# Kernel tuning notes

Hardware: AMD Instinct MI355X
Metric: run time of the kernel (lower is better)

## Reference

```python
import jax, jax.numpy as jnp
import numpy as np

N_ITERATIONS = 3
EPS = 1e-07


def squash(t, axis=-1):
    sqr_norm = jnp.sum(t * t, axis=axis, keepdims=True)
    norm = jnp.sqrt(sqr_norm + EPS)
    return sqr_norm * t / ((1.0 + sqr_norm) * norm)


def setup_inputs() -> dict:
    key = jax.random.key(0)
    B, N_IN, N_OUT, D = 256, 1152, 10, 16
    u_hat = jax.random.normal(key, (B, N_IN, N_OUT, D, 1), dtype=jnp.float32)
    return {"u_hat": u_hat}


def reference(u_hat):
    # u_hat: [B, n_in, n_out, d, 1]
    B, n_in, n_out = u_hat.shape[0], u_hat.shape[1], u_hat.shape[2]
    b = jnp.zeros((B, n_in, n_out, 1, 1), dtype=u_hat.dtype)
    v = None
    for r in range(N_ITERATIONS):
        c = jax.nn.softmax(b, axis=1)                      # softmax over input caps
        s = jnp.sum(c * u_hat, axis=1, keepdims=True)      # [B, 1, n_out, d, 1]
        v = squash(s, axis=-2)                             # squash over capsule dim
        if r < N_ITERATIONS - 1:
            # u_hat^T @ v (broadcast v over input caps): agreement [B, n_in, n_out, 1, 1]
            a = jnp.sum(u_hat * v, axis=-2, keepdims=True)
            b = b + a
    return jnp.squeeze(v, axis=1)                          # [B, n_out, d, 1]
```

## Files before the change

kernel.cpp:

```cpp
#include <hip/hip_runtime.h>

#define BATCH 256
#define NIN   1152
#define NOUT  10
#define DDIM  16
#define KPT   18

__global__ __launch_bounds__(256)
void routing_kernel(const float* __restrict__ u_hat, float* __restrict__ out) {
    __shared__ float bsh[NIN];
    __shared__ float wsh[NIN];
    __shared__ float red[4 * DDIM];
    __shared__ float vsh[DDIM];
    __shared__ float scal[8];

    const int t    = threadIdx.x;
    const int q    = t & 3;
    const int g    = t >> 2;
    const int wave = t >> 6;
    const int lane = t & 63;

    const int x   = blockIdx.x;
    const int xcd = x & 7;
    const int j   = x >> 3;
    const int oo  = j % NOUT;
    const int bb  = xcd * 32 + j / NOUT;

    const float* base = u_hat + (size_t)bb * (NIN * NOUT * DDIM) + oo * DDIM + q * 4;

    float4 u[KPT];
#pragma unroll
    for (int k = 0; k < KPT; ++k) {
        const int i = g + 64 * k;
        u[k] = *reinterpret_cast<const float4*>(base + (size_t)i * (NOUT * DDIM));
    }

    for (int i = t; i < NIN; i += 256) bsh[i] = 0.0f;
    __syncthreads();

    for (int r = 0; r < 3; ++r) {
        float m = -3.4e38f;
        for (int i = t; i < NIN; i += 256) m = fmaxf(m, bsh[i]);
        for (int off = 32; off >= 1; off >>= 1) m = fmaxf(m, __shfl_down(m, off));
        if (lane == 0) scal[wave] = m;
        __syncthreads();
        m = fmaxf(fmaxf(scal[0], scal[1]), fmaxf(scal[2], scal[3]));

        float z = 0.0f;
        for (int i = t; i < NIN; i += 256) {
            const float w = __expf(bsh[i] - m);
            wsh[i] = w;
            z += w;
        }
        for (int off = 32; off >= 1; off >>= 1) z += __shfl_down(z, off);
        if (lane == 0) scal[4 + wave] = z;
        __syncthreads();
        const float invZ = 1.0f / (scal[4] + scal[5] + scal[6] + scal[7]);

        float sx = 0.f, sy = 0.f, sz = 0.f, sw = 0.f;
#pragma unroll
        for (int k = 0; k < KPT; ++k) {
            const float w = wsh[g + 64 * k];
            sx += w * u[k].x; sy += w * u[k].y; sz += w * u[k].z; sw += w * u[k].w;
        }
        for (int off = 32; off >= 4; off >>= 1) {
            sx += __shfl_down(sx, off);
            sy += __shfl_down(sy, off);
            sz += __shfl_down(sz, off);
            sw += __shfl_down(sw, off);
        }
        if (lane < 4) {
            float* rp = &red[wave * DDIM + lane * 4];
            rp[0] = sx; rp[1] = sy; rp[2] = sz; rp[3] = sw;
        }
        __syncthreads();
        if (t < DDIM) {
            vsh[t] = (red[t] + red[DDIM + t] + red[2 * DDIM + t] + red[3 * DDIM + t]) * invZ;
        }
        __syncthreads();

        float sqr = 0.0f;
#pragma unroll
        for (int d = 0; d < DDIM; ++d) { const float sv = vsh[d]; sqr += sv * sv; }
        const float scale = sqr / ((1.0f + sqr) * sqrtf(sqr + 1e-7f));
        __syncthreads();
        if (t < DDIM) vsh[t] *= scale;
        __syncthreads();

        if (r == 2) break;

        const float vx = vsh[q * 4 + 0], vy = vsh[q * 4 + 1];
        const float vz = vsh[q * 4 + 2], vw = vsh[q * 4 + 3];
#pragma unroll
        for (int k = 0; k < KPT; ++k) {
            float a = u[k].x * vx + u[k].y * vy + u[k].z * vz + u[k].w * vw;
            a += __shfl_xor(a, 1);
            a += __shfl_xor(a, 2);
            if (q == 0) bsh[g + 64 * k] += a;
        }
        __syncthreads();
    }

    if (t < DDIM) {
        out[(size_t)(bb * NOUT + oo) * DDIM + t] = vsh[t];
    }
}

extern "C" void kernel_launch(void* const* d_in, const int* in_sizes, int n_in,
                              void* d_out, int out_size, void* d_ws, size_t ws_size,
                              hipStream_t stream) {
    const float* u_hat = (const float*)d_in[0];
    float* out = (float*)d_out;
    routing_kernel<<<dim3(BATCH * NOUT), dim3(256), 0, stream>>>(u_hat, out);
}
```

Before: 260.7 us.

## Give each thread whole capsule vectors and keep routing logits in registers

Each thread now owns whole 16-dim input-capsule vectors (5 or 4 capsules per thread) instead of a quarter-vector for 18 capsules. The routing logits and softmax weights stay in registers, which removes the shared-memory logit and weight arrays and several barriers. The cross-lane 16-wide sum uses a recursive-halving shuffle reduction. The trade is more registers per thread (up to 80 floats for u), uneven work between threads, and 64-byte strided loads per thread, which may coalesce less well.

```diff
diff --git a/kernel.cpp b/kernel.cpp
--- a/kernel.cpp
+++ b/kernel.cpp
@@ -1,22 +1,16 @@
 #include <hip/hip_runtime.h>
 
-#define BATCH 256
 #define NIN   1152
 #define NOUT  10
-#define DDIM  16
-#define KPT   18
+#define CMAX  5
 
 __global__ __launch_bounds__(256)
 void routing_kernel(const float* __restrict__ u_hat, float* __restrict__ out) {
-    __shared__ float bsh[NIN];
-    __shared__ float wsh[NIN];
-    __shared__ float red[4 * DDIM];
-    __shared__ float vsh[DDIM];
+    __shared__ float l2s[4][16];
+    __shared__ __align__(16) float vsh[16];
     __shared__ float scal[8];
 
     const int t    = threadIdx.x;
-    const int q    = t & 3;
-    const int g    = t >> 2;
     const int wave = t >> 6;
     const int lane = t & 63;
 
@@ -26,83 +20,134 @@
     const int oo  = j % NOUT;
     const int bb  = xcd * 32 + j / NOUT;
 
-    const float* base = u_hat + (size_t)bb * (NIN * NOUT * DDIM) + oo * DDIM + q * 4;
+    const int c = (t < 128) ? 5 : 4;
 
-    float4 u[KPT];
+    const float* base = u_hat + ((size_t)bb * NIN + t) * (NOUT * 16) + oo * 16;
+
+    float4 u[CMAX][4];
 #pragma unroll
-    for (int k = 0; k < KPT; ++k) {
-        const int i = g + 64 * k;
-        u[k] = *reinterpret_cast<const float4*>(base + (size_t)i * (NOUT * DDIM));
+    for (int k = 0; k < CMAX; ++k) {
+        if (k < c) {
+            const float* rp = base + (size_t)k * 256 * (NOUT * 16);
+            u[k][0] = *reinterpret_cast<const float4*>(rp);
+            u[k][1] = *reinterpret_cast<const float4*>(rp + 4);
+            u[k][2] = *reinterpret_cast<const float4*>(rp + 8);
+            u[k][3] = *reinterpret_cast<const float4*>(rp + 12);
+        }
     }
 
-    for (int i = t; i < NIN; i += 256) bsh[i] = 0.0f;
-    __syncthreads();
+    float b[CMAX] = {0.f, 0.f, 0.f, 0.f, 0.f};
 
     for (int r = 0; r < 3; ++r) {
-        float m = -3.4e38f;
-        for (int i = t; i < NIN; i += 256) m = fmaxf(m, bsh[i]);
+        float m = b[0];
+#pragma unroll
+        for (int k = 1; k < CMAX; ++k) if (k < c) m = fmaxf(m, b[k]);
         for (int off = 32; off >= 1; off >>= 1) m = fmaxf(m, __shfl_down(m, off));
         if (lane == 0) scal[wave] = m;
         __syncthreads();
-        m = fmaxf(fmaxf(scal[0], scal[1]), fmaxf(scal[2], scal[3]));
+        const float M = fmaxf(fmaxf(scal[0], scal[1]), fmaxf(scal[2], scal[3]));
 
-        float z = 0.0f;
-        for (int i = t; i < NIN; i += 256) {
-            const float w = __expf(bsh[i] - m);
-            wsh[i] = w;
-            z += w;
+        float e[CMAX];
+        float z = 0.f;
+#pragma unroll
+        for (int k = 0; k < CMAX; ++k) {
+            if (k < c) { e[k] = __expf(b[k] - M); z += e[k]; }
         }
         for (int off = 32; off >= 1; off >>= 1) z += __shfl_down(z, off);
         if (lane == 0) scal[4 + wave] = z;
         __syncthreads();
         const float invZ = 1.0f / (scal[4] + scal[5] + scal[6] + scal[7]);
 
-        float sx = 0.f, sy = 0.f, sz = 0.f, sw = 0.f;
+        float A[16];
 #pragma unroll
-        for (int k = 0; k < KPT; ++k) {
-            const float w = wsh[g + 64 * k];
-            sx += w * u[k].x; sy += w * u[k].y; sz += w * u[k].z; sw += w * u[k].w;
+        for (int d = 0; d < 16; ++d) A[d] = 0.f;
+#pragma unroll
+        for (int k = 0; k < CMAX; ++k) {
+            if (k < c) {
+                const float w = e[k];
+                A[ 0] += w * u[k][0].x; A[ 1] += w * u[k][0].y;
+                A[ 2] += w * u[k][0].z; A[ 3] += w * u[k][0].w;
+                A[ 4] += w * u[k][1].x; A[ 5] += w * u[k][1].y;
+                A[ 6] += w * u[k][1].z; A[ 7] += w * u[k][1].w;
+                A[ 8] += w * u[k][2].x; A[ 9] += w * u[k][2].y;
+                A[10] += w * u[k][2].z; A[11] += w * u[k][2].w;
+                A[12] += w * u[k][3].x; A[13] += w * u[k][3].y;
+                A[14] += w * u[k][3].z; A[15] += w * u[k][3].w;
+            }
         }
-        for (int off = 32; off >= 4; off >>= 1) {
-            sx += __shfl_down(sx, off);
-            sy += __shfl_down(sy, off);
-            sz += __shfl_down(sz, off);
-            sw += __shfl_down(sw, off);
+
+        {
+            const bool hi = (lane & 32) != 0;
+#pragma unroll
+            for (int i = 0; i < 8; ++i) {
+                const float snd = hi ? A[i] : A[i + 8];
+                const float rcv = __shfl_xor(snd, 32);
+                A[i] = (hi ? A[i + 8] : A[i]) + rcv;
+            }
         }
-        if (lane < 4) {
-            float* rp = &red[wave * DDIM + lane * 4];
-            rp[0] = sx; rp[1] = sy; rp[2] = sz; rp[3] = sw;
+        {
+            const bool hi = (lane & 16) != 0;
+#pragma unroll
+            for (int i = 0; i < 4; ++i) {
+                const float snd = hi ? A[i] : A[i + 4];
+                const float rcv = __shfl_xor(snd, 16);
+                A[i] = (hi ? A[i + 4] : A[i]) + rcv;
+            }
         }
+        {
+            const bool hi = (lane & 8) != 0;
+#pragma unroll
+            for (int i = 0; i < 2; ++i) {
+                const float snd = hi ? A[i] : A[i + 2];
+                const float rcv = __shfl_xor(snd, 8);
+                A[i] = (hi ? A[i + 2] : A[i]) + rcv;
+            }
+        }
+        {
+            const bool hi = (lane & 4) != 0;
+            const float snd = hi ? A[1] : A[1];
+            const float snd2 = hi ? A[0] : A[1];
+            (void)snd;
+            const float rcv = __shfl_xor(snd2, 4);
+            A[0] = (hi ? A[1] : A[0]) + rcv;
+        }
+        A[0] += __shfl_xor(A[0], 2);
+        A[0] += __shfl_xor(A[0], 1);
+        if ((lane & 3) == 0) l2s[wave][lane >> 2] = A[0];
         __syncthreads();
-        if (t < DDIM) {
-            vsh[t] = (red[t] + red[DDIM + t] + red[2 * DDIM + t] + red[3 * DDIM + t]) * invZ;
+
+        if (t < 16) {
+            vsh[t] = (l2s[0][t] + l2s[1][t] + l2s[2][t] + l2s[3][t]) * invZ;
         }
         __syncthreads();
 
-        float sqr = 0.0f;
+        const float4 s0 = *reinterpret_cast<const float4*>(&vsh[0]);
+        const float4 s1 = *reinterpret_cast<const float4*>(&vsh[4]);
+        const float4 s2 = *reinterpret_cast<const float4*>(&vsh[8]);
+        const float4 s3 = *reinterpret_cast<const float4*>(&vsh[12]);
+        const float sqr =
+            s0.x*s0.x + s0.y*s0.y + s0.z*s0.z + s0.w*s0.w +
+            s1.x*s1.x + s1.y*s1.y + s1.z*s1.z + s1.w*s1.w +
+            s2.x*s2.x + s2.y*s2.y + s2.z*s2.z + s2.w*s2.w +
+            s3.x*s3.x + s3.y*s3.y + s3.z*s3.z + s3.w*s3.w;
+        const float scale = sqr / ((1.0f + sqr) * sqrtf(sqr + 1e-7f));
+
+        if (r == 2) {
+            if (t < 16) out[(size_t)(bb * NOUT + oo) * 16 + t] = vsh[t] * scale;
+            break;
+        }
+
 #pragma unroll
-        for (int d = 0; d < DDIM; ++d) { const float sv = vsh[d]; sqr += sv * sv; }
-        const float scale = sqr / ((1.0f + sqr) * sqrtf(sqr + 1e-7f));
-        __syncthreads();
-        if (t < DDIM) vsh[t] *= scale;
-        __syncthreads();
-
-        if (r == 2) break;
-
-        const float vx = vsh[q * 4 + 0], vy = vsh[q * 4 + 1];
-        const float vz = vsh[q * 4 + 2], vw = vsh[q * 4 + 3];
-#pragma unroll
-        for (int k = 0; k < KPT; ++k) {
-            float a = u[k].x * vx + u[k].y * vy + u[k].z * vz + u[k].w * vw;
-            a += __shfl_xor(a, 1);
-            a += __shfl_xor(a, 2);
-            if (q == 0) bsh[g + 64 * k] += a;
+        for (int k = 0; k < CMAX; ++k) {
+            if (k < c) {
+                const float dot =
+                    u[k][0].x*s0.x + u[k][0].y*s0.y + u[k][0].z*s0.z + u[k][0].w*s0.w +
+                    u[k][1].x*s1.x + u[k][1].y*s1.y + u[k][1].z*s1.z + u[k][1].w*s1.w +
+                    u[k][2].x*s2.x + u[k][2].y*s2.y + u[k][2].z*s2.z + u[k][2].w*s2.w +
+                    u[k][3].x*s3.x + u[k][3].y*s3.y + u[k][3].z*s3.z + u[k][3].w*s3.w;
+                b[k] += dot * scale;
+            }
         }
-        __syncthreads();
-    }
-
-    if (t < DDIM) {
-        out[(size_t)(bb * NOUT + oo) * DDIM + t] = vsh[t];
     }
 }
 
@@ -111,5 +156,5 @@
                               hipStream_t stream) {
     const float* u_hat = (const float*)d_in[0];
     float* out = (float*)d_out;
-    routing_kernel<<<dim3(BATCH * NOUT), dim3(256), 0, stream>>>(u_hat, out);
+    routing_kernel<<<dim3(256 * NOUT), dim3(256), 0, stream>>>(u_hat, out);
 }
```

Result: slower. 268.1 us (+2.8%).
